# Optimization experiments

Hardware: AMD Instinct MI355X
Metric: run time of the kernel (lower is better)

Reference implementation:

```python
import math
import jax, jax.numpy as jnp
import numpy as np

HIDDEN = 1024
HEADS = 16
HEAD_DIM = HIDDEN // HEADS
PRIME = 7
MAX_ITERS = 10
ENT_THRESH = 0.2
PRIME_SCALE = 1.0 / math.sqrt(PRIME * HEAD_DIM)
EPS = 1e-6


def setup_inputs() -> dict:
    key = jax.random.key(0)
    ks = jax.random.split(key, 6)
    B, S = 2, 2048
    w = 0.02
    return {
        "hidden_states": jax.random.normal(ks[0], (B, S, HIDDEN), jnp.float32),
        "q_w": jax.random.normal(ks[1], (HIDDEN, HIDDEN), jnp.float32) * w,
        "q_b": jnp.zeros((HIDDEN,), jnp.float32),
        "k_w": jax.random.normal(ks[2], (HIDDEN, HIDDEN), jnp.float32) * w,
        "k_b": jnp.zeros((HIDDEN,), jnp.float32),
        "v_w": jax.random.normal(ks[3], (HIDDEN, HIDDEN), jnp.float32) * w,
        "v_b": jnp.zeros((HIDDEN,), jnp.float32),
        "o_w": jax.random.normal(ks[4], (HIDDEN, HIDDEN), jnp.float32) * w,
        "o_b": jnp.zeros((HIDDEN,), jnp.float32),
        "attention_mask": jnp.ones((B, S), jnp.int32),
    }


def _split_heads(x):
    B, S, _ = x.shape
    return x.reshape(B, S, HEADS, HEAD_DIM).transpose(0, 2, 1, 3)


def reference(hidden_states, q_w, q_b, k_w, k_b, v_w, v_b, o_w, o_b, attention_mask):
    B, S, _ = hidden_states.shape
    # projections (torch Linear: x @ W^T + b)
    q = _split_heads(hidden_states @ q_w.T + q_b) * PRIME_SCALE  # [B,H,S,hd]
    k = _split_heads(hidden_states @ k_w.T + k_b)
    v = _split_heads(hidden_states @ v_w.T + v_b)

    scores = jnp.einsum("bhqd,bhkd->bhqk", q, k)  # [B,H,S,S]
    mask = attention_mask[:, None, None, :]
    scores = jnp.where(mask == 0, -jnp.inf, scores)
    attn = jax.nn.softmax(scores, axis=-1)  # dropout p=0 (eval)

    base = jnp.einsum("bhqk,bhkd->bhqd", attn, v)  # attention_weights @ v

    # entropy of the (fixed) attention weights: [B,H]
    entropy = -jnp.sum(attn * jnp.log(attn + EPS), axis=-1).mean(axis=-1)
    avg_entropy = entropy.mean()

    # loop never changes attn, so entropy is constant: either break at i=1 or run all
    full = base
    for i in range(1, MAX_ITERS):
        blend = 1.0 / (1.0 + math.exp(-i / MAX_ITERS))          # sigmoid(i/max)
        res_scale = 0.5 + 0.5 * blend                            # resonance scale
        full = (1.0 - blend) * full + blend * (res_scale * base)

    out_heads = jnp.where(avg_entropy < ENT_THRESH, base, full)  # [B,H,S,hd]

    merged = out_heads.transpose(0, 2, 1, 3).reshape(B, S, HIDDEN)
    return merged @ o_w.T + o_b
```

## Files before the change

### kernel.cpp

```cpp
#include <hip/hip_runtime.h>
#include <hip/hip_bf16.h>
#include <stdint.h>


#define PRIME_SCALE 0.047245559126654356f
#define LOG2E       1.4426950408889634f
#define LN2         0.6931471805599453f
#define QSCALE      (PRIME_SCALE * LOG2E)
#define BLEND_C     0.85096556f

#if __has_builtin(__builtin_amdgcn_exp2f)
#define EXP2(x) __builtin_amdgcn_exp2f(x)
#else
#define EXP2(x) exp2f(x)
#endif

typedef __attribute__((ext_vector_type(8))) short short8;
typedef __attribute__((ext_vector_type(4))) float f32x4;

__device__ __forceinline__ unsigned short f2bf(float x) {
    union { float f; unsigned int u; } v; v.f = x;
    unsigned int r = (v.u + 0x7fffu + ((v.u >> 16) & 1u)) >> 16;
    return (unsigned short)r;
}
__device__ __forceinline__ unsigned short f2bf_fast(float x) {
    union { float f; unsigned int u; } v; v.f = x;
    return (unsigned short)((v.u + 0x8000u) >> 16);
}
__device__ __forceinline__ float bf2f(unsigned short x) {
    union { unsigned int u; float f; } v; v.u = ((unsigned int)x) << 16;
    return v.f;
}
__device__ __forceinline__ unsigned cvtpk_bf16(float lo, float hi) {
    unsigned r;
    asm("v_cvt_pk_bf16_f32 %0, %1, %2" : "=v"(r) : "v"(lo), "v"(hi));
    return r;
}

__device__ __forceinline__ void glds16(const unsigned short* g, unsigned short* l) {
    __builtin_amdgcn_global_load_lds((const __attribute__((address_space(1))) unsigned int*)g,
                                     (__attribute__((address_space(3))) unsigned int*)l,
                                     16, 0, 0);
}

__global__ void zero_out_f32(float* p, int n) {
    int i = blockIdx.x * 256 + threadIdx.x;
    if (i < n) p[i] = 0.f;
}

__global__ __launch_bounds__(256) void cvt5(
    const float* __restrict__ s0, const float* __restrict__ s1, const float* __restrict__ s2,
    const float* __restrict__ s3, const float* __restrict__ s4,
    unsigned short* __restrict__ d0, unsigned short* __restrict__ d1, unsigned short* __restrict__ d2,
    unsigned short* __restrict__ d3, unsigned short* __restrict__ d4, float* entp)
{
    if (blockIdx.x == 0 && threadIdx.x == 0) entp[0] = 0.f;
    unsigned int i = blockIdx.x * 256 + threadIdx.x;
    const float* s; unsigned short* d; unsigned int off;
    if (i < (1u << 20)) { s = s0; d = d0; off = i; }
    else {
        unsigned int j = i - (1u << 20);
        unsigned int sel = j >> 18; off = j & 0x3FFFFu;
        s = sel == 0 ? s1 : sel == 1 ? s2 : sel == 2 ? s3 : s4;
        d = sel == 0 ? d1 : sel == 1 ? d2 : sel == 2 ? d3 : d4;
    }
    float4 v = ((const float4*)s)[off];
    ushort4 p; p.x = f2bf(v.x); p.y = f2bf(v.y); p.z = f2bf(v.z); p.w = f2bf(v.w);
    ((ushort4*)d)[off] = p;
}

__global__ __launch_bounds__(256) void gemm_qkv(
    const unsigned short* __restrict__ hsb,
    const unsigned short* __restrict__ qwb, const unsigned short* __restrict__ kwb,
    const unsigned short* __restrict__ vwb,
    const float* __restrict__ qb, const float* __restrict__ kb, const float* __restrict__ vb,
    unsigned short* __restrict__ Qo, unsigned short* __restrict__ Ko, unsigned short* __restrict__ Vto)
{
    const int bid = blockIdx.x;
    const int x = bid & 7;
    const int i = bid >> 3;
    const int op = i >> 5;
    const int j = i & 31;
    const unsigned short *A, *B; const float* bias; unsigned short* C;
    int m0, n0, ldc, biasRow; float scale;
    if (op == 0)      { A = hsb; B = qwb; bias = qb; C = Qo;
                        m0 = (x * 4 + (j >> 3)) * 128; n0 = (j & 7) * 128;  ldc = 1024; biasRow = 0; scale = QSCALE; }
    else if (op == 1) { A = hsb; B = kwb; bias = kb; C = Ko;
                        m0 = (x * 4 + (j >> 3)) * 128; n0 = (j & 7) * 128;  ldc = 1024; biasRow = 0; scale = 1.f; }
    else              { A = vwb; B = hsb; bias = vb; C = Vto;
                        m0 = (j & 7) * 128; n0 = (x * 4 + (j >> 3)) * 128;  ldc = 4096; biasRow = 1; scale = 1.f; }

    __shared__ unsigned short As[128 * 32];
    __shared__ unsigned short Bs[128 * 32];
    const int t = threadIdx.x, lane = t & 63, w = t >> 6;
    const int quad = lane >> 4, l15 = lane & 15;
    const int wr = (w >> 1) * 64, wc = (w & 1) * 64;
    const int srow = lane >> 2, scol = (lane & 3) * 8;

    f32x4 acc[4][4];
#pragma unroll
    for (int ii = 0; ii < 4; ++ii)
#pragma unroll
        for (int jj = 0; jj < 4; ++jj) acc[ii][jj] = (f32x4){0.f, 0.f, 0.f, 0.f};

    for (int kk = 0; kk < 32; ++kk) {
        const int k0 = kk * 32;
#pragma unroll
        for (int jj = 0; jj < 2; ++jj) {
            int row = (w * 2 + jj) * 16 + srow;
            glds16(&A[(size_t)(m0 + row) * 1024 + k0 + scol], &As[(w * 2 + jj) * 512]);
            glds16(&B[(size_t)(n0 + row) * 1024 + k0 + scol], &Bs[(w * 2 + jj) * 512]);
        }
        __syncthreads();
        short8 af[4], bf[4];
#pragma unroll
        for (int mt = 0; mt < 4; ++mt) af[mt] = *(const short8*)&As[(wr + mt * 16 + l15) * 32 + quad * 8];
#pragma unroll
        for (int nt = 0; nt < 4; ++nt) bf[nt] = *(const short8*)&Bs[(wc + nt * 16 + l15) * 32 + quad * 8];
#pragma unroll
        for (int mt = 0; mt < 4; ++mt)
#pragma unroll
            for (int nt = 0; nt < 4; ++nt)
                acc[mt][nt] = __builtin_amdgcn_mfma_f32_16x16x32_bf16(af[mt], bf[nt], acc[mt][nt], 0, 0, 0);
        __syncthreads();
    }
#pragma unroll
    for (int mt = 0; mt < 4; ++mt) {
#pragma unroll
        for (int nt = 0; nt < 4; ++nt) {
            int n = n0 + wc + nt * 16 + l15;
#pragma unroll
            for (int r = 0; r < 4; ++r) {
                int m = m0 + wr + mt * 16 + quad * 4 + r;
                float bval = biasRow ? bias[m] : bias[n];
                C[(size_t)m * ldc + n] = f2bf((acc[mt][nt][r] + bval) * scale);
            }
        }
    }
}


#define STAGE(KT, BUF) do {                                                         \
    int kn_ = (KT) * 64;                                                            \
    _Pragma("unroll")                                                               \
    for (int i_ = 0; i_ < 2; ++i_) {                                                \
        int row_ = w * 16 + i_ * 8 + r8;                                            \
        int c_ = ch8 ^ (row_ & 7);                                                  \
        glds16(&K[(size_t)(b * 2048 + kn_ + row_) * 1024 + h * 64 + c_ * 8],        \
               &Ks[BUF][(w * 16 + i_ * 8) * 64]);                                   \
        glds16(&Vt[(size_t)(h * 64 + row_) * 4096 + b * 2048 + kn_ + c_ * 8],       \
               &Vs[BUF][(w * 16 + i_ * 8) * 64]);                                   \
    }                                                                               \
} while (0)

#define QK_SOFTMAX(MASKED)                                                          \
    _Pragma("unroll")                                                               \
    for (int nt = 0; nt < 4; ++nt) {                                                \
        int krow = nt * 16 + l15;                                                   \
        short8 kf0 = *(const short8*)&Ks[cur][krow * 64 + ((quad ^ (krow & 7)) * 8)];       \
        short8 kf1 = *(const short8*)&Ks[cur][krow * 64 + (((quad + 4) ^ (krow & 7)) * 8)]; \
        f32x4 sv[2];                                                                \
        __builtin_amdgcn_s_setprio(1);                                              \
        _Pragma("unroll")                                                           \
        for (int st = 0; st < 2; ++st) {                                            \
            sv[st] = __builtin_amdgcn_mfma_f32_16x16x32_bf16(kf0, qa[st][0], (f32x4){0.f, 0.f, 0.f, 0.f}, 0, 0, 0); \
            sv[st] = __builtin_amdgcn_mfma_f32_16x16x32_bf16(kf1, qa[st][1], sv[st], 0, 0, 0); \
        }                                                                           \
        __builtin_amdgcn_s_setprio(0);                                              \
        unsigned mb = 0xFu;                                                         \
        if (MASKED) {                                                               \
            unsigned mw = (nt & 2) ? mwB : mwA;                                     \
            mb = (mw >> (((nt & 1) << 4) + (quad << 2))) & 0xFu;                    \
        }                                                                           \
        _Pragma("unroll")                                                           \
        for (int st = 0; st < 2; ++st) {                                            \
            float s0 = sv[st][0], s1 = sv[st][1], s2 = sv[st][2], s3 = sv[st][3];   \
            if (MASKED) {                                                           \
                s0 = (mb & 1u) ? s0 : -1.0e30f;                                     \
                s1 = (mb & 2u) ? s1 : -1.0e30f;                                     \
                s2 = (mb & 4u) ? s2 : -1.0e30f;                                     \
                s3 = (mb & 8u) ? s3 : -1.0e30f;                                     \
            }                                                                       \
            float p0 = EXP2(s0), p1 = EXP2(s1), p2 = EXP2(s2), p3 = EXP2(s3);       \
            l_r[st] += (p0 + p1) + (p2 + p3);                                       \
            T_r[st] += (p0 * s0 + p1 * s1) + (p2 * s2 + p3 * s3);                   \
            pk[nt][st][0] = cvtpk_bf16(p0, p1);                                     \
            pk[nt][st][1] = cvtpk_bf16(p2, p3);                                     \
        }                                                                           \
    }

__global__ __launch_bounds__(256, 2) void flash_full(
    const unsigned short* __restrict__ Q,
    const unsigned short* __restrict__ K,
    const unsigned short* __restrict__ Vt,
    const int* __restrict__ mask,
    unsigned short* __restrict__ O,
    float* __restrict__ entp)
{
    const int ww = ((blockIdx.x & 7) << 6) + (blockIdx.x >> 3);
    const int qt = ww & 15;
    const int bh = ww >> 4;
    const int b = bh >> 4, h = bh & 15;
    const int t = threadIdx.x, lane = t & 63, w = t >> 6;
    const int quad = lane >> 4, l15 = lane & 15;
    const int r8 = lane >> 3, ch8 = lane & 7;

    __shared__ __align__(16) unsigned short Ks[2][64 * 64];
    __shared__ __align__(16) unsigned short Vs[2][64 * 64];
    __shared__ unsigned int maskBits[64];
    __shared__ float went[4];

    short8 qa[2][2];
#pragma unroll
    for (int st = 0; st < 2; ++st) {
        size_t qrow = (size_t)(b * 2048 + qt * 128 + w * 32 + st * 16 + l15) * 1024 + h * 64;
        union { uint4 v; short8 s8; } u0, u1;
        u0.v = *(const uint4*)&Q[qrow + quad * 8];
        u1.v = *(const uint4*)&Q[qrow + 32 + quad * 8];
        qa[st][0] = u0.s8; qa[st][1] = u1.s8;
    }

    {
        const int4* mp = (const int4*)(mask + b * 2048 + t * 8);
        int4 a = mp[0], c = mp[1];
        unsigned bits = (unsigned)(a.x != 0)       | ((unsigned)(a.y != 0) << 1)
                      | ((unsigned)(a.z != 0) << 2) | ((unsigned)(a.w != 0) << 3)
                      | ((unsigned)(c.x != 0) << 4) | ((unsigned)(c.y != 0) << 5)
                      | ((unsigned)(c.z != 0) << 6) | ((unsigned)(c.w != 0) << 7);
        ((unsigned char*)maskBits)[t] = (unsigned char)bits;
    }

    STAGE(0, 0);
    STAGE(1, 1);

    float l_r[2] = {0.f, 0.f}, T_r[2] = {0.f, 0.f};
    f32x4 o_acc[2][4];
#pragma unroll
    for (int st = 0; st < 2; ++st)
#pragma unroll
        for (int nt = 0; nt < 4; ++nt) o_acc[st][nt] = (f32x4){0.f, 0.f, 0.f, 0.f};

    asm volatile("s_waitcnt lgkmcnt(0)" ::: "memory");
    asm volatile("s_waitcnt vmcnt(4)" ::: "memory");
    asm volatile("s_barrier" ::: "memory");

    for (int kt = 0; kt < 32; ++kt) {
        const int cur = kt & 1;
        unsigned mwA = maskBits[kt * 2], mwB = maskBits[kt * 2 + 1];

        unsigned pk[4][2][2];
        if ((mwA & mwB) == 0xFFFFFFFFu) {
            QK_SOFTMAX(0)
        } else {
            QK_SOFTMAX(1)
        }

#pragma unroll
        for (int ks = 0; ks < 2; ++ks) {
            short8 pa[2];
#pragma unroll
            for (int st = 0; st < 2; ++st) {
                unsigned a0 = pk[2 * ks][st][0], a1 = pk[2 * ks][st][1];
                unsigned b0 = pk[2 * ks + 1][st][0], b1 = pk[2 * ks + 1][st][1];
                asm("v_permlane32_swap_b32 %0, %1" : "+v"(a0), "+v"(b0));
                asm("v_permlane32_swap_b32 %0, %1" : "+v"(a1), "+v"(b1));
                asm("v_permlane16_swap_b32 %0, %1" : "+v"(a0), "+v"(b0));
                asm("v_permlane16_swap_b32 %0, %1" : "+v"(a1), "+v"(b1));
                union { unsigned u[4]; short8 s8; } uu;
                uu.u[0] = a0; uu.u[1] = a1; uu.u[2] = b0; uu.u[3] = b1;
                pa[st] = uu.s8;
            }
            __builtin_amdgcn_s_setprio(1);
#pragma unroll
            for (int nt = 0; nt < 4; ++nt) {
                int vrow = nt * 16 + l15;
                short8 vf = *(const short8*)&Vs[cur][vrow * 64 + ((((ks * 4 + quad)) ^ (vrow & 7)) * 8)];
#pragma unroll
                for (int st = 0; st < 2; ++st)
                    o_acc[st][nt] = __builtin_amdgcn_mfma_f32_16x16x32_bf16(pa[st], vf, o_acc[st][nt], 0, 0, 0);
            }
            __builtin_amdgcn_s_setprio(0);
        }

        if (kt < 31) {
            asm volatile("s_barrier" ::: "memory");
            if (kt < 30) {
                STAGE(kt + 2, cur);
                asm volatile("s_waitcnt vmcnt(4)" ::: "memory");
            } else {
                asm volatile("s_waitcnt vmcnt(0)" ::: "memory");
            }
            asm volatile("s_barrier" ::: "memory");
        }
    }

    float ent_acc = 0.f;
#pragma unroll
    for (int st = 0; st < 2; ++st) {
        float l = l_r[st], T = T_r[st];
        l += __shfl_xor(l, 16); T += __shfl_xor(T, 16);
        l += __shfl_xor(l, 32); T += __shfl_xor(T, 32);
        ent_acc += __log2f(l) - T / l;
        float inv[4];
#pragma unroll
        for (int r = 0; r < 4; ++r)
            inv[r] = 1.0f / __shfl(l, quad * 4 + r);
#pragma unroll
        for (int r = 0; r < 4; ++r) {
            int mrow = b * 2048 + qt * 128 + w * 32 + st * 16 + quad * 4 + r;
#pragma unroll
            for (int nt = 0; nt < 4; ++nt)
                O[(size_t)mrow * 1024 + h * 64 + nt * 16 + l15] = f2bf_fast(o_acc[st][nt][r] * inv[r]);
        }
    }
    ent_acc += __shfl_xor(ent_acc, 1);
    ent_acc += __shfl_xor(ent_acc, 2);
    ent_acc += __shfl_xor(ent_acc, 4);
    ent_acc += __shfl_xor(ent_acc, 8);
    if (lane == 0) went[w] = ent_acc;
    __syncthreads();
    if (t == 0)
        atomicAdd(entp, LN2 * (went[0] + went[1] + went[2] + went[3]));
}

__global__ __launch_bounds__(256) void gemm_out_bf(
    const unsigned short* __restrict__ A, const unsigned short* __restrict__ Bw,
    const float* __restrict__ bias, const float* __restrict__ entp,
    float* __restrict__ C)
{
    const float avg = entp[0] * (1.0f / 65536.0f);
    const float scale = (avg < 0.2f) ? 1.0f : BLEND_C;

    const int x = blockIdx.x & 7;
    const int j = blockIdx.x >> 3;
    const int m0 = (x * 4 + (j >> 4)) * 128;
    const int n0 = (j & 15) * 64;
    __shared__ unsigned short As[128 * 32];
    __shared__ unsigned short Bs[64 * 32];
    const int t = threadIdx.x, lane = t & 63, w = t >> 6;
    const int quad = lane >> 4, l15 = lane & 15;
    const int wr = (w >> 1) * 64, wc = (w & 1) * 32;
    const int srow = lane >> 2, scol = (lane & 3) * 8;

    f32x4 acc[4][2];
#pragma unroll
    for (int ii = 0; ii < 4; ++ii)
#pragma unroll
        for (int jj = 0; jj < 2; ++jj) acc[ii][jj] = (f32x4){0.f, 0.f, 0.f, 0.f};

    for (int kk = 0; kk < 32; ++kk) {
        const int k0 = kk * 32;
#pragma unroll
        for (int jj = 0; jj < 2; ++jj) {
            int row = (w * 2 + jj) * 16 + srow;
            glds16(&A[(size_t)(m0 + row) * 1024 + k0 + scol], &As[(w * 2 + jj) * 512]);
        }
        {
            int row = w * 16 + srow;
            glds16(&Bw[(size_t)(n0 + row) * 1024 + k0 + scol], &Bs[w * 512]);
        }
        __syncthreads();
        short8 af[4], bf[2];
#pragma unroll
        for (int mt = 0; mt < 4; ++mt) af[mt] = *(const short8*)&As[(wr + mt * 16 + l15) * 32 + quad * 8];
#pragma unroll
        for (int nt = 0; nt < 2; ++nt) bf[nt] = *(const short8*)&Bs[(wc + nt * 16 + l15) * 32 + quad * 8];
#pragma unroll
        for (int mt = 0; mt < 4; ++mt)
#pragma unroll
            for (int nt = 0; nt < 2; ++nt)
                acc[mt][nt] = __builtin_amdgcn_mfma_f32_16x16x32_bf16(af[mt], bf[nt], acc[mt][nt], 0, 0, 0);
        __syncthreads();
    }
#pragma unroll
    for (int mt = 0; mt < 4; ++mt) {
#pragma unroll
        for (int nt = 0; nt < 2; ++nt) {
            int n = n0 + wc + nt * 16 + l15;
#pragma unroll
            for (int r = 0; r < 4; ++r) {
                int m = m0 + wr + mt * 16 + quad * 4 + r;
                C[(size_t)m * 1024 + n] = scale * acc[mt][nt][r] + bias[n];
            }
        }
    }
}

extern "C" void kernel_launch(void* const* d_in, const int* in_sizes, int n_in,
                              void* d_out, int out_size, void* d_ws, size_t ws_size,
                              hipStream_t stream)
{
    const float* hs = (const float*)d_in[0];
    const float* qw = (const float*)d_in[1];
    const float* qb = (const float*)d_in[2];
    const float* kw = (const float*)d_in[3];
    const float* kb = (const float*)d_in[4];
    const float* vw = (const float*)d_in[5];
    const float* vb = (const float*)d_in[6];
    const float* ow = (const float*)d_in[7];
    const float* ob = (const float*)d_in[8];
    const int*   mask = (const int*)d_in[9];
    float* out = (float*)d_out;

    const size_t MB = 1024 * 1024;
    char* ws = (char*)d_ws;
    dim3 blk(256);

    if (ws_size >= 50 * MB) {
        unsigned short* hsb = (unsigned short*)(ws);
        unsigned short* Q   = (unsigned short*)(ws + 8 * MB);
        unsigned short* Kp  = (unsigned short*)(ws + 16 * MB);
        unsigned short* Vt  = (unsigned short*)(ws + 24 * MB);
        unsigned short* qwb = (unsigned short*)(ws + 32 * MB);
        unsigned short* kwb = (unsigned short*)(ws + 34 * MB);
        unsigned short* vwb = (unsigned short*)(ws + 36 * MB);
        unsigned short* owb = (unsigned short*)(ws + 38 * MB);
        float* entp         = (float*)(ws + 40 * MB);
        unsigned short* O   = hsb;

        cvt5<<<dim3(8192), blk, 0, stream>>>(hs, qw, kw, vw, ow, hsb, qwb, kwb, vwb, owb, entp);
        gemm_qkv<<<dim3(768), blk, 0, stream>>>(hsb, qwb, kwb, vwb, qb, kb, vb, Q, Kp, Vt);
        flash_full<<<dim3(512), blk, 0, stream>>>(Q, Kp, Vt, mask, O, entp);
        gemm_out_bf<<<dim3(512), blk, 0, stream>>>(O, owb, ob, entp, out);
    } else {
        zero_out_f32<<<dim3((out_size + 255) / 256), blk, 0, stream>>>(out, out_size);
    }
}
```

Before: 202.8 us.

## Deepen K/V LDS pipeline to four stages and process two tiles per barrier

After: 202.8 us. About the same (+0.0%).

```diff
diff --git a/kernel.cpp b/kernel.cpp
--- a/kernel.cpp
+++ b/kernel.cpp
@@ -147,18 +147,18 @@
         int row_ = w * 16 + i_ * 8 + r8;                                            \
         int c_ = ch8 ^ (row_ & 7);                                                  \
         glds16(&K[(size_t)(b * 2048 + kn_ + row_) * 1024 + h * 64 + c_ * 8],        \
-               &Ks[BUF][(w * 16 + i_ * 8) * 64]);                                   \
+               &Ks[(BUF) * 4096 + (w * 16 + i_ * 8) * 64]);                         \
         glds16(&Vt[(size_t)(h * 64 + row_) * 4096 + b * 2048 + kn_ + c_ * 8],       \
-               &Vs[BUF][(w * 16 + i_ * 8) * 64]);                                   \
+               &Vs[(BUF) * 4096 + (w * 16 + i_ * 8) * 64]);                         \
     }                                                                               \
 } while (0)
 
-#define QK_SOFTMAX(MASKED)                                                          \
+#define QK_SOFTMAX(MASKED, Kb, mwA, mwB)                                            \
     _Pragma("unroll")                                                               \
     for (int nt = 0; nt < 4; ++nt) {                                                \
         int krow = nt * 16 + l15;                                                   \
-        short8 kf0 = *(const short8*)&Ks[cur][krow * 64 + ((quad ^ (krow & 7)) * 8)];       \
-        short8 kf1 = *(const short8*)&Ks[cur][krow * 64 + (((quad + 4) ^ (krow & 7)) * 8)]; \
+        short8 kf0 = *(const short8*)&(Kb)[krow * 64 + ((quad ^ (krow & 7)) * 8)];       \
+        short8 kf1 = *(const short8*)&(Kb)[krow * 64 + (((quad + 4) ^ (krow & 7)) * 8)]; \
         f32x4 sv[2];                                                                \
         __builtin_amdgcn_s_setprio(1);                                              \
         _Pragma("unroll")                                                           \
@@ -169,7 +169,7 @@
         __builtin_amdgcn_s_setprio(0);                                              \
         unsigned mb = 0xFu;                                                         \
         if (MASKED) {                                                               \
-            unsigned mw = (nt & 2) ? mwB : mwA;                                     \
+            unsigned mw = (nt & 2) ? (mwB) : (mwA);                                 \
             mb = (mw >> (((nt & 1) << 4) + (quad << 2))) & 0xFu;                    \
         }                                                                           \
         _Pragma("unroll")                                                           \
@@ -189,6 +189,44 @@
         }                                                                           \
     }
 
+#define TILE_BODY(KT, BUF) do {                                                     \
+    unsigned mwA = maskBits[(KT) * 2], mwB = maskBits[(KT) * 2 + 1];                \
+    const unsigned short* Kb = Ks + (BUF) * 4096;                                   \
+    const unsigned short* Vb = Vs + (BUF) * 4096;                                   \
+    unsigned pk[4][2][2];                                                           \
+    if ((mwA & mwB) == 0xFFFFFFFFu) {                                               \
+        QK_SOFTMAX(0, Kb, mwA, mwB)                                                 \
+    } else {                                                                        \
+        QK_SOFTMAX(1, Kb, mwA, mwB)                                                 \
+    }                                                                               \
+    _Pragma("unroll")                                                               \
+    for (int ks = 0; ks < 2; ++ks) {                                                \
+        short8 pa[2];                                                               \
+        _Pragma("unroll")                                                           \
+        for (int st = 0; st < 2; ++st) {                                            \
+            unsigned a0 = pk[2 * ks][st][0], a1 = pk[2 * ks][st][1];                \
+            unsigned b0 = pk[2 * ks + 1][st][0], b1 = pk[2 * ks + 1][st][1];        \
+            asm("v_permlane32_swap_b32 %0, %1" : "+v"(a0), "+v"(b0));               \
+            asm("v_permlane32_swap_b32 %0, %1" : "+v"(a1), "+v"(b1));               \
+            asm("v_permlane16_swap_b32 %0, %1" : "+v"(a0), "+v"(b0));               \
+            asm("v_permlane16_swap_b32 %0, %1" : "+v"(a1), "+v"(b1));               \
+            union { unsigned u[4]; short8 s8; } uu;                                 \
+            uu.u[0] = a0; uu.u[1] = a1; uu.u[2] = b0; uu.u[3] = b1;                 \
+            pa[st] = uu.s8;                                                         \
+        }                                                                           \
+        __builtin_amdgcn_s_setprio(1);                                              \
+        _Pragma("unroll")                                                           \
+        for (int nt = 0; nt < 4; ++nt) {                                            \
+            int vrow = nt * 16 + l15;                                               \
+            short8 vf = *(const short8*)&Vb[vrow * 64 + ((((ks * 4 + quad)) ^ (vrow & 7)) * 8)]; \
+            _Pragma("unroll")                                                       \
+            for (int st = 0; st < 2; ++st)                                          \
+                o_acc[st][nt] = __builtin_amdgcn_mfma_f32_16x16x32_bf16(pa[st], vf, o_acc[st][nt], 0, 0, 0); \
+        }                                                                           \
+        __builtin_amdgcn_s_setprio(0);                                              \
+    }                                                                               \
+} while (0)
+
 __global__ __launch_bounds__(256, 2) void flash_full(
     const unsigned short* __restrict__ Q,
     const unsigned short* __restrict__ K,
@@ -205,8 +243,8 @@
     const int quad = lane >> 4, l15 = lane & 15;
     const int r8 = lane >> 3, ch8 = lane & 7;
 
-    __shared__ __align__(16) unsigned short Ks[2][64 * 64];
-    __shared__ __align__(16) unsigned short Vs[2][64 * 64];
+    __shared__ __align__(16) unsigned short Ks[4 * 64 * 64];
+    __shared__ __align__(16) unsigned short Vs[4 * 64 * 64];
     __shared__ unsigned int maskBits[64];
     __shared__ float went[4];
 
@@ -232,6 +270,8 @@
 
     STAGE(0, 0);
     STAGE(1, 1);
+    STAGE(2, 2);
+    STAGE(3, 3);
 
     float l_r[2] = {0.f, 0.f}, T_r[2] = {0.f, 0.f};
     f32x4 o_acc[2][4];
@@ -241,52 +281,20 @@
         for (int nt = 0; nt < 4; ++nt) o_acc[st][nt] = (f32x4){0.f, 0.f, 0.f, 0.f};
 
     asm volatile("s_waitcnt lgkmcnt(0)" ::: "memory");
-    asm volatile("s_waitcnt vmcnt(4)" ::: "memory");
+    asm volatile("s_waitcnt vmcnt(8)" ::: "memory");
     asm volatile("s_barrier" ::: "memory");
 
-    for (int kt = 0; kt < 32; ++kt) {
-        const int cur = kt & 1;
-        unsigned mwA = maskBits[kt * 2], mwB = maskBits[kt * 2 + 1];
-
-        unsigned pk[4][2][2];
-        if ((mwA & mwB) == 0xFFFFFFFFu) {
-            QK_SOFTMAX(0)
-        } else {
-            QK_SOFTMAX(1)
-        }
-
-#pragma unroll
-        for (int ks = 0; ks < 2; ++ks) {
-            short8 pa[2];
-#pragma unroll
-            for (int st = 0; st < 2; ++st) {
-                unsigned a0 = pk[2 * ks][st][0], a1 = pk[2 * ks][st][1];
-                unsigned b0 = pk[2 * ks + 1][st][0], b1 = pk[2 * ks + 1][st][1];
-                asm("v_permlane32_swap_b32 %0, %1" : "+v"(a0), "+v"(b0));
-                asm("v_permlane32_swap_b32 %0, %1" : "+v"(a1), "+v"(b1));
-                asm("v_permlane16_swap_b32 %0, %1" : "+v"(a0), "+v"(b0));
-                asm("v_permlane16_swap_b32 %0, %1" : "+v"(a1), "+v"(b1));
-                union { unsigned u[4]; short8 s8; } uu;
-                uu.u[0] = a0; uu.u[1] = a1; uu.u[2] = b0; uu.u[3] = b1;
-                pa[st] = uu.s8;
-            }
-            __builtin_amdgcn_s_setprio(1);
-#pragma unroll
-            for (int nt = 0; nt < 4; ++nt) {
-                int vrow = nt * 16 + l15;
-                short8 vf = *(const short8*)&Vs[cur][vrow * 64 + ((((ks * 4 + quad)) ^ (vrow & 7)) * 8)];
-#pragma unroll
-                for (int st = 0; st < 2; ++st)
-                    o_acc[st][nt] = __builtin_amdgcn_mfma_f32_16x16x32_bf16(pa[st], vf, o_acc[st][nt], 0, 0, 0);
-            }
-            __builtin_amdgcn_s_setprio(0);
-        }
-
-        if (kt < 31) {
+    for (int kt = 0; kt < 32; kt += 2) {
+        const int b0 = kt & 3, b1 = (kt + 1) & 3;
+        TILE_BODY(kt, b0);
+        TILE_BODY(kt + 1, b1);
+
+        if (kt < 30) {
             asm volatile("s_barrier" ::: "memory");
-            if (kt < 30) {
-                STAGE(kt + 2, cur);
-                asm volatile("s_waitcnt vmcnt(4)" ::: "memory");
+            if (kt < 28) {
+                STAGE(kt + 4, b0);
+                STAGE(kt + 5, b1);
+                asm volatile("s_waitcnt vmcnt(8)" ::: "memory");
             } else {
                 asm volatile("s_waitcnt vmcnt(0)" ::: "memory");
             }
```
